# Kernel optimization log

Hardware: AMD Instinct MI355X
Metric: run time of the kernel (lower is better)

Reference implementation:

```python
import jax, jax.numpy as jnp
import numpy as np

NUM_CLASSES = 21
GAMMA = 2.0
LAMBDA_WGT = 0.1
EPS = 1e-6
D, H, W = 256, 512, 512


def setup_inputs() -> dict:
    key = jax.random.key(0)
    k1, k2, k3, k4, k5 = jax.random.split(key, 5)
    # probabilities in (0,1); avoid exact 0 so log is finite
    y_pred = jax.random.uniform(k1, (NUM_CLASSES, H, W), dtype=jnp.float32, minval=1e-4, maxval=1.0)
    ycrf = jax.random.randint(k2, (H, W), 0, NUM_CLASSES, dtype=jnp.int32)
    yret = jax.random.randint(k3, (H, W), 0, NUM_CLASSES, dtype=jnp.int32)
    feature_map = jax.random.normal(k4, (D, H, W), dtype=jnp.float32)
    classifier_weight = jax.random.normal(k5, (NUM_CLASSES, D), dtype=jnp.float32)
    return {"y_pred": y_pred, "ycrf": ycrf, "yret": yret,
            "feature_map": feature_map, "classifier_weight": classifier_weight}


def reference(y_pred, ycrf, yret, feature_map, classifier_weight):
    C = NUM_CLASSES
    logp = jnp.log(y_pred)                                   # [C,H,W]
    # gather log p at the CRF label per pixel
    logp_crf = jnp.take_along_axis(logp, ycrf[None].astype(jnp.int32), axis=0)[0]  # [H,W]
    s = (ycrf == yret)                                       # pixels where ycrf==yret==c (s_class union)
    s_f = s.astype(logp.dtype)

    # ---- loss_ce: -sum_{p: ycrf==yret} log p[ycrf(p), p] / count ----
    denom_ce = jnp.sum(s_f)
    numer_ce = jnp.sum(jnp.where(s, logp_crf, 0.0))
    loss_ce = -numer_ce / denom_ce

    # ---- correlation map: 1 + cos(feature_map, w_c) along channel dim ----
    f_norm = jnp.maximum(jnp.sqrt(jnp.sum(feature_map * feature_map, axis=0)), EPS)   # [H,W]
    w_norm = jnp.maximum(jnp.sqrt(jnp.sum(classifier_weight * classifier_weight, axis=1)), EPS)  # [C]
    dots = jnp.einsum('dhw,cd->chw', feature_map, classifier_weight)                  # [C,H,W]
    corr = 1.0 + dots / (w_norm[:, None, None] * f_norm[None])                        # [C,H,W]

    # c* map = corr at the CRF label; original max includes an all-zeros extra row
    corr_star = jnp.take_along_axis(corr, ycrf[None].astype(jnp.int32), axis=0)[0]    # [H,W]
    corr_max = jnp.maximum(jnp.max(corr, axis=0), 0.0)                                # [H,W]
    conf = (corr_star / corr_max) ** GAMMA                                            # [H,W]

    # ---- loss_wce: per class i, sum over pixels NOT in s_i of conf * log p_i ----
    # each pixel appears (C - 1{ycrf==yret}) times in denom; numer excludes class ycrf when s holds
    denom_w = jnp.sum(conf * (C - s_f))
    numer_w = jnp.sum(conf * (jnp.sum(logp, axis=0) - s_f * logp_crf))
    loss_wce = -numer_w / denom_w

    return (loss_ce + LAMBDA_WGT * loss_wce, loss_ce, loss_wce)
```

## Files before the change

kernel.cpp:

```cpp
#include <hip/hip_runtime.h>
#include <math.h>

#define NCLS 21
#define DD   256
#define HWPIX (512*512)
#define PIX  4
#define HW4  (HWPIX/PIX)
#define EPSV 1e-6f

#define WT_STRIDE 24
#define WT_FLOATS (DD*WT_STRIDE)
#define THREADS 256
#define MAIN_BLOCKS (HW4/THREADS)
#define UND 8

typedef float __attribute__((ext_vector_type(2))) f2;
typedef float __attribute__((ext_vector_type(4))) f4;
typedef int   __attribute__((ext_vector_type(4))) i4;

__global__ void prep_weights(const float* __restrict__ w,
                             float* __restrict__ wt)
{
    __shared__ float warr[4];
    __shared__ float inv_s;
    const int c = blockIdx.x, d = threadIdx.x;
    float v = w[c*DD + d];
    float s = v * v;
    #pragma unroll
    for (int off = 32; off; off >>= 1) s += __shfl_xor(s, off, 64);
    int wave = d >> 6, lane = d & 63;
    if (lane == 0) warr[wave] = s;
    __syncthreads();
    if (d == 0) inv_s = 1.0f / fmaxf(sqrtf(warr[0]+warr[1]+warr[2]+warr[3]), EPSV);
    __syncthreads();
    wt[d*WT_STRIDE + c] = v * inv_s;
}

__global__ __launch_bounds__(THREADS)
void main_kernel(const float* __restrict__ yp,
                 const int*   __restrict__ ycrf,
                 const int*   __restrict__ yret,
                 const float* __restrict__ fm,
                 const float* __restrict__ wt,
                 float* __restrict__ partials)
{
    __shared__ float lds_wt[WT_FLOATS];
    __shared__ float red[4][4];

    const int tid = threadIdx.x;

    {
        const f4* src = (const f4*)wt;
        f4* dst = (f4*)lds_wt;
        #pragma unroll
        for (int i = 0; i < WT_FLOATS/4/THREADS; ++i)
            dst[i*THREADS + tid] = src[i*THREADS + tid];
    }
    __syncthreads();

    const int g = blockIdx.x * THREADS + tid;
    const f4* fm4 = (const f4*)fm;
    const f4* yp4 = (const f4*)yp;
    const i4* yc4 = (const i4*)ycrf;
    const i4* yr4 = (const i4*)yret;

    f2 dotA[NCLS], dotB[NCLS];
    f2 nnA = {0.f, 0.f}, nnB = {0.f, 0.f};
    #pragma unroll
    for (int c = 0; c < NCLS; ++c) { dotA[c] = nnA; dotB[c] = nnA; }

    float wrA[24], wrB[24];
    {
        const f4* wr4 = (const f4*)&lds_wt[0];
        #pragma unroll
        for (int i = 0; i < 6; ++i) ((f4*)wrA)[i] = wr4[i];
    }

    f4 v[UND];
    #pragma unroll
    for (int u = 0; u < UND; ++u)
        v[u] = __builtin_nontemporal_load(&fm4[u*HW4 + g]);

    #define ROW(VV, WC, WN, DN)                                           \
        do {                                                              \
            const int _dn = (DN) & (DD - 1);                              \
            const f4* _wr4 = (const f4*)&lds_wt[_dn*WT_STRIDE];           \
            _Pragma("unroll")                                             \
            for (int i = 0; i < 6; ++i) ((f4*)(WN))[i] = _wr4[i];         \
            f2 _va = {(VV).x, (VV).y}, _vb = {(VV).z, (VV).w};            \
            _Pragma("unroll")                                             \
            for (int c = 0; c < NCLS; ++c) {                              \
                dotA[c] += _va * (WC)[c];                                 \
                dotB[c] += _vb * (WC)[c];                                 \
            }                                                             \
            nnA += _va * _va;                                             \
            nnB += _vb * _vb;                                             \
        } while (0)

    for (int d0 = 0; d0 < DD; d0 += UND) {
        f4 nv[UND];
        if (d0 + UND < DD) {
            #pragma unroll
            for (int u = 0; u < UND; ++u)
                nv[u] = __builtin_nontemporal_load(&fm4[(d0 + UND + u)*HW4 + g]);
        }
        ROW(v[0], wrA, wrB, d0 + 1);
        ROW(v[1], wrB, wrA, d0 + 2);
        ROW(v[2], wrA, wrB, d0 + 3);
        ROW(v[3], wrB, wrA, d0 + 4);
        ROW(v[4], wrA, wrB, d0 + 5);
        ROW(v[5], wrB, wrA, d0 + 6);
        ROW(v[6], wrA, wrB, d0 + 7);
        ROW(v[7], wrB, wrA, d0 + 8);
        #pragma unroll
        for (int u = 0; u < UND; ++u) v[u] = nv[u];
    }
    #undef ROW

    const i4 yc = yc4[g], yr = yr4[g];

    float conf[PIX];
    {
        float nn[PIX] = { nnA.x, nnA.y, nnB.x, nnB.y };
        int   yck[PIX] = { yc.x, yc.y, yc.z, yc.w };
        #pragma unroll
        for (int k = 0; k < PIX; ++k) {
            float inv_fn = 1.0f / fmaxf(sqrtf(nn[k]), EPSV);
            float cs = 0.f, cm = 0.f;
            #pragma unroll
            for (int c = 0; c < NCLS; ++c) {
                float d = (k == 0) ? dotA[c].x : (k == 1) ? dotA[c].y
                        : (k == 2) ? dotB[c].x : dotB[c].y;
                float cv = fmaf(d, inv_fn, 1.0f);
                cm = fmaxf(cm, cv);
                cs = (yck[k] == c) ? cv : cs;
            }
            float r = cs / cm;
            conf[k] = r * r;
        }
    }

    f4 p[NCLS];
    #pragma unroll
    for (int c = 0; c < NCLS; ++c)
        p[c] = __builtin_nontemporal_load(&yp4[c*HW4 + g]);

    float slp[PIX] = {0.f,0.f,0.f,0.f}, lpc[PIX] = {0.f,0.f,0.f,0.f};
    {
        int yck[PIX] = { yc.x, yc.y, yc.z, yc.w };
        #pragma unroll
        for (int c = 0; c < NCLS; ++c) {
            float l0 = __logf(p[c].x), l1 = __logf(p[c].y);
            float l2 = __logf(p[c].z), l3 = __logf(p[c].w);
            slp[0] += l0; slp[1] += l1; slp[2] += l2; slp[3] += l3;
            lpc[0] = (yck[0] == c) ? l0 : lpc[0];
            lpc[1] = (yck[1] == c) ? l1 : lpc[1];
            lpc[2] = (yck[2] == c) ? l2 : lpc[2];
            lpc[3] = (yck[3] == c) ? l3 : lpc[3];
        }
    }

    float a_nce = 0.f, a_dce = 0.f, a_dw = 0.f, a_nw = 0.f;
    {
        int yck[PIX] = { yc.x, yc.y, yc.z, yc.w };
        int yrk[PIX] = { yr.x, yr.y, yr.z, yr.w };
        #pragma unroll
        for (int k = 0; k < PIX; ++k) {
            bool s = (yck[k] == yrk[k]);
            float sf = s ? 1.f : 0.f;
            float sl = s ? lpc[k] : 0.f;
            a_nce += sl;
            a_dce += sf;
            a_dw  += conf[k] * ((float)NCLS - sf);
            a_nw  += conf[k] * (slp[k] - sl);
        }
    }

    #pragma unroll
    for (int off = 32; off; off >>= 1) {
        a_nce += __shfl_xor(a_nce, off, 64);
        a_dce += __shfl_xor(a_dce, off, 64);
        a_dw  += __shfl_xor(a_dw,  off, 64);
        a_nw  += __shfl_xor(a_nw,  off, 64);
    }
    int wave = tid >> 6, lane = tid & 63;
    if (lane == 0) { red[wave][0]=a_nce; red[wave][1]=a_dce; red[wave][2]=a_dw; red[wave][3]=a_nw; }
    __syncthreads();
    if (tid == 0) {
        #pragma unroll
        for (int i = 0; i < 4; ++i)
            partials[blockIdx.x*4 + i] = red[0][i] + red[1][i] + red[2][i] + red[3][i];
    }
}

__global__ void finalize(const float* __restrict__ partials, float* __restrict__ out)
{
    __shared__ float red[4][4];
    int tid = threadIdx.x;
    float s[4] = {0.f, 0.f, 0.f, 0.f};
    for (int b = tid; b < MAIN_BLOCKS; b += THREADS) {
        #pragma unroll
        for (int i = 0; i < 4; ++i) s[i] += partials[b*4 + i];
    }
    #pragma unroll
    for (int off = 32; off; off >>= 1) {
        #pragma unroll
        for (int i = 0; i < 4; ++i) s[i] += __shfl_xor(s[i], off, 64);
    }
    int wave = tid >> 6, lane = tid & 63;
    if (lane == 0) { red[wave][0]=s[0]; red[wave][1]=s[1]; red[wave][2]=s[2]; red[wave][3]=s[3]; }
    __syncthreads();
    if (tid == 0) {
        float nce = red[0][0]+red[1][0]+red[2][0]+red[3][0];
        float dce = red[0][1]+red[1][1]+red[2][1]+red[3][1];
        float dw  = red[0][2]+red[1][2]+red[2][2]+red[3][2];
        float nw  = red[0][3]+red[1][3]+red[2][3]+red[3][3];
        float ce  = -nce / dce;
        float wce = -nw  / dw;
        out[0] = ce + 0.1f * wce;
        out[1] = ce;
        out[2] = wce;
    }
}

extern "C" void kernel_launch(void* const* d_in, const int* in_sizes, int n_in,
                              void* d_out, int out_size, void* d_ws, size_t ws_size,
                              hipStream_t stream) {
    const float* y_pred = (const float*)d_in[0];
    const int*   ycrf   = (const int*)d_in[1];
    const int*   yret   = (const int*)d_in[2];
    const float* fmap   = (const float*)d_in[3];
    const float* cw     = (const float*)d_in[4];
    float* out = (float*)d_out;

    float* wt       = (float*)d_ws;
    float* partials = wt + WT_FLOATS;

    prep_weights<<<NCLS, THREADS, 0, stream>>>(cw, wt);
    main_kernel<<<MAIN_BLOCKS, THREADS, 0, stream>>>(y_pred, ycrf, yret, fmap, wt, partials);
    finalize<<<1, THREADS, 0, stream>>>(partials, out);
}
```

Measured before the change: 73.46 us.

## Interleave y_pred loads and log reduction into the feature-map channel loop

The 21 class-probability loads move out of the kernel tail. They are now issued in three chunks of seven, with each chunk's logs consumed at fixed points inside the channel-dot loop, so the y_pred traffic overlaps the feature-map streaming. Previously all y_pred loads were issued only after the dot-product phase had finished. The label loads are hoisted to the start. The launch bounds are set to one block per CU, which allows more registers but may cut occupancy.

```diff
diff --git a/kernel.cpp b/kernel.cpp
--- a/kernel.cpp
+++ b/kernel.cpp
@@ -36,7 +36,7 @@
     wt[d*WT_STRIDE + c] = v * inv_s;
 }
 
-__global__ __launch_bounds__(THREADS)
+__global__ __launch_bounds__(THREADS, 1)
 void main_kernel(const float* __restrict__ yp,
                  const int*   __restrict__ ycrf,
                  const int*   __restrict__ yret,
@@ -64,11 +64,38 @@
     const i4* yc4 = (const i4*)ycrf;
     const i4* yr4 = (const i4*)yret;
 
+    const i4 yc = yc4[g], yr = yr4[g];
+    const int yck[PIX] = { yc.x, yc.y, yc.z, yc.w };
+
     f2 dotA[NCLS], dotB[NCLS];
     f2 nnA = {0.f, 0.f}, nnB = {0.f, 0.f};
     #pragma unroll
     for (int c = 0; c < NCLS; ++c) { dotA[c] = nnA; dotB[c] = nnA; }
 
+    float slp[PIX] = {0.f,0.f,0.f,0.f}, lpc[PIX] = {0.f,0.f,0.f,0.f};
+    f4 pch[7];
+
+    #define YP_ISSUE(BASE)                                                \
+        do {                                                              \
+            _Pragma("unroll")                                             \
+            for (int c = 0; c < 7; ++c)                                   \
+                pch[c] = __builtin_nontemporal_load(&yp4[((BASE)+c)*HW4 + g]); \
+        } while (0)
+
+    #define YP_CONSUME(BASE)                                              \
+        do {                                                              \
+            _Pragma("unroll")                                             \
+            for (int c = 0; c < 7; ++c) {                                 \
+                float l0 = __logf(pch[c].x), l1 = __logf(pch[c].y);       \
+                float l2 = __logf(pch[c].z), l3 = __logf(pch[c].w);       \
+                slp[0] += l0; slp[1] += l1; slp[2] += l2; slp[3] += l3;   \
+                lpc[0] = (yck[0] == (BASE)+c) ? l0 : lpc[0];              \
+                lpc[1] = (yck[1] == (BASE)+c) ? l1 : lpc[1];              \
+                lpc[2] = (yck[2] == (BASE)+c) ? l2 : lpc[2];              \
+                lpc[3] = (yck[3] == (BASE)+c) ? l3 : lpc[3];              \
+            }                                                             \
+        } while (0)
+
     float wrA[24], wrB[24];
     {
         const f4* wr4 = (const f4*)&lds_wt[0];
@@ -80,6 +107,8 @@
     #pragma unroll
     for (int u = 0; u < UND; ++u)
         v[u] = __builtin_nontemporal_load(&fm4[u*HW4 + g]);
+
+    YP_ISSUE(0);
 
     #define ROW(VV, WC, WN, DN)                                           \
         do {                                                              \
@@ -97,6 +126,7 @@
             nnB += _vb * _vb;                                             \
         } while (0)
 
+    #pragma unroll 1
     for (int d0 = 0; d0 < DD; d0 += UND) {
         f4 nv[UND];
         if (d0 + UND < DD) {
@@ -104,6 +134,8 @@
             for (int u = 0; u < UND; ++u)
                 nv[u] = __builtin_nontemporal_load(&fm4[(d0 + UND + u)*HW4 + g]);
         }
+        if (d0 == 64)  { YP_CONSUME(0);  YP_ISSUE(7);  }
+        if (d0 == 128) { YP_CONSUME(7);  YP_ISSUE(14); }
         ROW(v[0], wrA, wrB, d0 + 1);
         ROW(v[1], wrB, wrA, d0 + 2);
         ROW(v[2], wrA, wrB, d0 + 3);
@@ -117,12 +149,11 @@
     }
     #undef ROW
 
-    const i4 yc = yc4[g], yr = yr4[g];
+    YP_CONSUME(14);
 
     float conf[PIX];
     {
         float nn[PIX] = { nnA.x, nnA.y, nnB.x, nnB.y };
-        int   yck[PIX] = { yc.x, yc.y, yc.z, yc.w };
         #pragma unroll
         for (int k = 0; k < PIX; ++k) {
             float inv_fn = 1.0f / fmaxf(sqrtf(nn[k]), EPSV);
@@ -140,29 +171,8 @@
         }
     }
 
-    f4 p[NCLS];
-    #pragma unroll
-    for (int c = 0; c < NCLS; ++c)
-        p[c] = __builtin_nontemporal_load(&yp4[c*HW4 + g]);
-
-    float slp[PIX] = {0.f,0.f,0.f,0.f}, lpc[PIX] = {0.f,0.f,0.f,0.f};
-    {
-        int yck[PIX] = { yc.x, yc.y, yc.z, yc.w };
-        #pragma unroll
-        for (int c = 0; c < NCLS; ++c) {
-            float l0 = __logf(p[c].x), l1 = __logf(p[c].y);
-            float l2 = __logf(p[c].z), l3 = __logf(p[c].w);
-            slp[0] += l0; slp[1] += l1; slp[2] += l2; slp[3] += l3;
-            lpc[0] = (yck[0] == c) ? l0 : lpc[0];
-            lpc[1] = (yck[1] == c) ? l1 : lpc[1];
-            lpc[2] = (yck[2] == c) ? l2 : lpc[2];
-            lpc[3] = (yck[3] == c) ? l3 : lpc[3];
-        }
-    }
-
     float a_nce = 0.f, a_dce = 0.f, a_dw = 0.f, a_nw = 0.f;
     {
-        int yck[PIX] = { yc.x, yc.y, yc.z, yc.w };
         int yrk[PIX] = { yr.x, yr.y, yr.z, yr.w };
         #pragma unroll
         for (int k = 0; k < PIX; ++k) {
```

Result: slower. 76.99 us (+4.8%).
